# Kernel tuning notes

Hardware: AMD Instinct MI355X
Metric: run time of the kernel (lower is better)

## Reference

```python
import jax, jax.numpy as jnp
import numpy as np


def setup_inputs() -> dict:
    key = jax.random.key(0)
    k1, k2, k3, k4, k5 = jax.random.split(key, 5)
    B, S, T = 256, 512, 64
    emissions = jax.random.normal(k1, (B, S, T), dtype=jnp.float32)
    tags = jax.random.randint(k2, (B, S), 0, T, dtype=jnp.int64)
    mask = jnp.ones((B, S), dtype=jnp.int32)
    init_range = 0.1
    start_transitions = jax.random.uniform(k3, (T,), minval=-init_range, maxval=init_range, dtype=jnp.float32)
    end_transitions = jax.random.uniform(k4, (T,), minval=-init_range, maxval=init_range, dtype=jnp.float32)
    transitions = jax.random.uniform(k5, (T, T), minval=-init_range, maxval=init_range, dtype=jnp.float32)
    return {"emissions": emissions, "tags": tags, "mask": mask,
            "start_transitions": start_transitions,
            "end_transitions": end_transitions,
            "transitions": transitions}


def _crf_nll_mean(emissions, tags, mask, start_transitions, end_transitions, transitions):
    # batch_first -> time-major: [S, B, T], [S, B]
    em = jnp.transpose(emissions, (1, 0, 2))
    tg = jnp.transpose(tags, (1, 0))
    mk = jnp.transpose(mask, (1, 0))
    maskf = mk.astype(em.dtype)                      # [S, B]
    S, B, T = em.shape
    batch_idx = jnp.arange(B)

    # ---- numerator: score of the gold path (fully vectorized) ----
    emit = jnp.take_along_axis(em, tg[:, :, None], axis=2)[..., 0]   # [S, B]
    trans_sc = transitions[tg[:-1], tg[1:]]                          # [S-1, B]
    score_num = start_transitions[tg[0]] + emit[0]
    score_num = score_num + jnp.sum((trans_sc + emit[1:]) * maskf[1:], axis=0)
    seq_ends = jnp.sum(mk, axis=0) - 1                               # [B]
    last_tags = tg[seq_ends, batch_idx]
    score_num = score_num + end_transitions[last_tags]

    # ---- denominator: log-partition via logsumexp scan ----
    init = start_transitions + em[0]                                 # [B, T]

    def step(score, xs):
        em_i, m_i = xs                                               # [B,T], [B]
        # [B, T_prev, T_next]
        next_score = score[:, :, None] + transitions[None, :, :] + em_i[:, None, :]
        next_score = jax.nn.logsumexp(next_score, axis=1)
        score = jnp.where(m_i[:, None] != 0, next_score, score)
        return score, None

    final, _ = jax.lax.scan(step, init, (em[1:], mk[1:]))
    denom = jax.nn.logsumexp(final + end_transitions, axis=1)        # [B]

    llh = denom - score_num                                          # [B]
    return jnp.mean(llh)                                             # reduction='mean'


def reference(emissions, tags, mask, start_transitions, end_transitions, transitions):
    return _crf_nll_mean(emissions, tags, mask, start_transitions, end_transitions, transitions)
```

## Files before the change

### kernel.cpp

```cpp
#include <hip/hip_runtime.h>

#define BATCH 256
#define SEQ   512
#define NT    64
#define PITCH 68

typedef __attribute__((ext_vector_type(8)))  short bf16x8;
typedef __attribute__((ext_vector_type(16))) float f32x16;
typedef __attribute__((ext_vector_type(4)))  float f32x4;
typedef __attribute__((ext_vector_type(2)))  float f32x2;

static __device__ __forceinline__ unsigned pk_bf16(float lo, float hi) {
    return __builtin_amdgcn_perm(__float_as_uint(hi), __float_as_uint(lo), 0x07060302u);
}
static __device__ __forceinline__ short bf16_trunc(float v) {
    return (short)(__float_as_uint(v) >> 16);
}

template<int CLEN_>
struct slice_bytes {
    static constexpr int v = (CLEN_ * NT * 4 > 64 * PITCH * 2) ? CLEN_ * NT * 4 : 64 * PITCH * 2;
};

template<int PCH_, int CLEN_>
static __device__ __forceinline__ void chunk_wave(
    const float* __restrict__ emissions,
    const float* __restrict__ trans,
    unsigned short* __restrict__ mats,
    unsigned char* slice,
    int b, int c, int lane)
{
    float*          w_flat = (float*)slice;
    unsigned short* ldsT   = (unsigned short*)slice;

    const int h  = lane >> 5;
    const int ml = lane & 31;

    const int s0 = c * CLEN_;
    int L = (SEQ - 1) - s0; if (L > CLEN_) L = CLEN_;

    const float* em_b = emissions + (size_t)b * SEQ * NT;

    {
        const float4* src = (const float4*)(em_b + (size_t)(s0 + 1) * NT);
        float4*       dst = (float4*)w_flat;
        const int total4 = L * (NT / 4);
        for (int i = lane; i < total4; i += 64) {
            float4 v = src[i];
            v.x = __expf(v.x); v.y = __expf(v.y);
            v.z = __expf(v.z); v.w = __expf(v.w);
            dst[i] = v;
        }
    }

    bf16x8 Af[2][4];
#pragma unroll
    for (int mt = 0; mt < 2; ++mt) {
        int m = mt * 32 + ml;
#pragma unroll
        for (int kk = 0; kk < 4; ++kk) {
            bf16x8 f;
#pragma unroll
            for (int j = 0; j < 8; ++j) {
                int r = 32 * (kk >> 1) + 16 * (kk & 1) + (j & 3) + 8 * (j >> 2) + 4 * h;
                f[j] = bf16_trunc(__expf(trans[r * NT + m]) * 0.0078125f);
            }
            Af[mt][kk] = f;
        }
    }

    union BU { unsigned u[4]; bf16x8 v; };
    BU Bv[4][2];
#pragma unroll
    for (int kk = 0; kk < 4; ++kk)
#pragma unroll
        for (int nt = 0; nt < 2; ++nt) {
            int n = nt * 32 + ml;
#pragma unroll
            for (int d = 0; d < 4; ++d) {
                int j0 = 2 * d;
                int r0 = 32 * (kk >> 1) + 16 * (kk & 1) + (j0 & 3) + 8 * (j0 >> 2) + 4 * h;
                unsigned lo = (r0     == n) ? 0x3f80u : 0u;
                unsigned hi = (r0 + 1 == n) ? 0x3f80u : 0u;
                Bv[kk][nt].u[d] = lo | (hi << 16);
            }
        }

    __threadfence_block();

    const f32x16 zf = {};

    for (int s = 0; s < L; ++s) {
        const float* wrow = w_flat + s * NT;
        f32x4 wq[4][2];
#pragma unroll
        for (int kk = 0; kk < 4; ++kk) {
            int base = 32 * (kk >> 1) + 16 * (kk & 1) + 4 * h;
            wq[kk][0] = *(const f32x4*)(wrow + base);
            wq[kk][1] = *(const f32x4*)(wrow + base + 8);
        }

#pragma unroll
        for (int nt = 0; nt < 2; ++nt) {
            __builtin_amdgcn_s_setprio(1);
            f32x16 a0 = __builtin_amdgcn_mfma_f32_32x32x16_bf16(Af[0][0], Bv[0][nt].v, zf, 0, 0, 0);
            f32x16 a1 = __builtin_amdgcn_mfma_f32_32x32x16_bf16(Af[1][0], Bv[0][nt].v, zf, 0, 0, 0);
#pragma unroll
            for (int kk = 1; kk < 4; ++kk) {
                a0 = __builtin_amdgcn_mfma_f32_32x32x16_bf16(Af[0][kk], Bv[kk][nt].v, a0, 0, 0, 0);
                a1 = __builtin_amdgcn_mfma_f32_32x32x16_bf16(Af[1][kk], Bv[kk][nt].v, a1, 0, 0, 0);
            }
            __builtin_amdgcn_s_setprio(0);

#pragma unroll
            for (int kk = 0; kk < 4; ++kk) {
                const int qo = 8 * (kk & 1);
                const f32x4 wa = wq[kk][0], wb = wq[kk][1];
#pragma unroll
                for (int d = 0; d < 4; ++d) {
                    const int j0 = 2 * d;
                    float w0 = (d < 2) ? wa[j0]     : wb[j0 - 4];
                    float w1 = (d < 2) ? wa[j0 + 1] : wb[j0 - 3];
                    f32x2 av, wv;
                    if (kk < 2) { av[0] = a0[qo + j0]; av[1] = a0[qo + j0 + 1]; }
                    else        { av[0] = a1[qo + j0]; av[1] = a1[qo + j0 + 1]; }
                    wv[0] = w0; wv[1] = w1;
                    f32x2 p = av * wv;
                    Bv[kk][nt].u[d] = pk_bf16(p[0], p[1]);
                }
            }
        }
    }

    __threadfence_block();
#pragma unroll
    for (int kk = 0; kk < 4; ++kk)
#pragma unroll
        for (int nt = 0; nt < 2; ++nt) {
            int n = nt * 32 + ml;
#pragma unroll
            for (int d = 0; d < 4; ++d) {
                int j0 = 2 * d;
                int r0 = 32 * (kk >> 1) + 16 * (kk & 1) + (j0 & 3) + 8 * (j0 >> 2) + 4 * h;
                *(unsigned*)&ldsT[n * PITCH + r0] = Bv[kk][nt].u[d];
            }
        }
    __threadfence_block();

    unsigned short* outp = mats + ((size_t)(b * PCH_ + c)) * 4096;
    for (int it = 0; it < 8; ++it) {
        int o = it * 512 + lane * 8;
        int n = o >> 6, k = o & 63;
        const uint2* p = (const uint2*)(ldsT + n * PITCH + k);
        uint2 x = p[0], y = p[1];
        uint4 q4; q4.x = x.x; q4.y = x.y; q4.z = y.x; q4.w = y.y;
        *(uint4*)(outp + o) = q4;
    }
}

template<int PCH_, int CLEN_>
__global__ __launch_bounds__(256, 3) void crf_chunk_packed(
    const float* __restrict__ emissions,
    const float* __restrict__ trans,
    unsigned short* __restrict__ mats,
    float* __restrict__ ws_head)
{
    constexpr int SLICE_B = slice_bytes<CLEN_>::v;
    __shared__ __align__(16) unsigned char smem[4 * SLICE_B];

    const int tid  = threadIdx.x;
    const int lane = tid & 63;
    const int wave = tid >> 6;
    const int b    = blockIdx.y;
    const int c    = blockIdx.x * 4 + wave;

    if (blockIdx.x == 0 && b == 0 && tid == 0) {
        ws_head[0] = 0.f;
        ((unsigned*)ws_head)[1] = 0u;
    }

    chunk_wave<PCH_, CLEN_>(emissions, trans, mats, smem + wave * SLICE_B, b, c, lane);
}

template<int PCH_, int CLEN_>
__global__ __launch_bounds__(64, 3) void crf_chunk_kernel(
    const float* __restrict__ emissions,
    const float* __restrict__ trans,
    unsigned short* __restrict__ mats,
    float* __restrict__ ws_head)
{
    constexpr int SMEM = slice_bytes<CLEN_>::v;
    __shared__ __align__(16) unsigned char smem[SMEM];

    const int c    = blockIdx.x;
    const int b    = blockIdx.y;
    const int lane = threadIdx.x;

    if (c == 0 && b == 0 && lane == 0) {
        ws_head[0] = 0.f;
        ((unsigned*)ws_head)[1] = 0u;
    }

    chunk_wave<PCH_, CLEN_>(emissions, trans, mats, smem, b, c, lane);
}

template<int PCH_>
__global__ __launch_bounds__(256) void crf_combine_kernel(
    const float* __restrict__ emissions,
    const int*   __restrict__ tags,
    const int*   __restrict__ mask,
    const float* __restrict__ start_tr,
    const float* __restrict__ end_tr,
    const float* __restrict__ trans,
    const unsigned short* __restrict__ mats,
    float* __restrict__ ws_head,
    float* __restrict__ out)
{
    __shared__ __align__(16) float r_lds[NT];
    __shared__ float score_lds;

    const int b    = blockIdx.x;
    const int tid  = threadIdx.x;
    const int j    = tid & 63;
    const int wave = tid >> 6;

    const float* em_b = emissions + (size_t)b * SEQ * NT;
    const int*   tg_b = tags + b * SEQ;
    const int*   mk_b = mask + b * SEQ;
    const unsigned short* mb = mats + (size_t)b * PCH_ * 4096;

    float denom = 0.f;

    if (wave >= 2) {
        const uint4* p = (const uint4*)mb;
        unsigned acc = 0;
        for (int i = (wave - 2) * 64 + j; i < PCH_ * 512; i += 128) {
            uint4 q = p[i];
            acc += q.x + q.y + q.z + q.w;
        }
        if (acc == 0xdeadbeefu) ws_head[2] = -1.f;
    } else if (wave == 1) {
        float part = 0.f;
        int mcount = 0;
        for (int s = j; s < SEQ; s += 64) {
            int m = mk_b[s];
            mcount += m;
            int t = tg_b[s];
            if (s == 0) {
                part += start_tr[t] + em_b[t];
            } else {
                int tp = tg_b[s - 1];
                float v = trans[tp * NT + t] + em_b[s * NT + t];
                part += m ? v : 0.f;
            }
        }
#pragma unroll
        for (int d = 32; d; d >>= 1) {
            part   += __shfl_xor(part, d);
            mcount += __shfl_xor(mcount, d);
        }
        if (j == 0) score_lds = part + end_tr[tg_b[mcount - 1]];
    } else {
        float r = __expf(end_tr[j]);
        r_lds[j] = r;
        __threadfence_block();
        int X = 0;

        uint4 cur[8], nxt[8];
#pragma unroll
        for (int u = 0; u < 8; ++u)
            cur[u] = *(const uint4*)(mb + (size_t)(PCH_ - 1) * 4096 + j * 64 + u * 8);

        for (int c = PCH_ - 1; c >= 0; --c) {
            if (c > 0) {
#pragma unroll
                for (int u = 0; u < 8; ++u)
                    nxt[u] = *(const uint4*)(mb + (size_t)(c - 1) * 4096 + j * 64 + u * 8);
            }
            float a0 = 0.f, a1 = 0.f, a2 = 0.f, a3 = 0.f;
#pragma unroll
            for (int u = 0; u < 8; ++u) {
                uint4 q = cur[u];
                f32x4 ra = *(const f32x4*)&r_lds[u * 8];
                f32x4 rb = *(const f32x4*)&r_lds[u * 8 + 4];
                a0 = fmaf(ra[0], __uint_as_float(q.x << 16),         a0);
                a1 = fmaf(ra[1], __uint_as_float(q.x & 0xffff0000u), a1);
                a2 = fmaf(ra[2], __uint_as_float(q.y << 16),         a2);
                a3 = fmaf(ra[3], __uint_as_float(q.y & 0xffff0000u), a3);
                a0 = fmaf(rb[0], __uint_as_float(q.z << 16),         a0);
                a1 = fmaf(rb[1], __uint_as_float(q.z & 0xffff0000u), a1);
                a2 = fmaf(rb[2], __uint_as_float(q.w << 16),         a2);
                a3 = fmaf(rb[3], __uint_as_float(q.w & 0xffff0000u), a3);
            }
            float rn = (a0 + a1) + (a2 + a3);
            unsigned eb = (__builtin_amdgcn_readfirstlane((int)__float_as_uint(rn)) >> 23) & 0xffu;
            r = rn * __uint_as_float((254u - eb) << 23);
            X += (int)eb - 127;
            r_lds[j] = r;
            __threadfence_block();
#pragma unroll
            for (int u = 0; u < 8; ++u) cur[u] = nxt[u];
        }

        float u0 = __expf(start_tr[j] + em_b[j]);
        float v = r * u0;
#pragma unroll
        for (int d = 32; d; d >>= 1) v += __shfl_xor(v, d);
        denom = __logf(v) + (float)(X + 7 * (SEQ - 1)) * 0.6931471805599453f;
    }

    __syncthreads();

    if (wave == 0 && j == 0) {
        float llh = denom - score_lds;
        atomicAdd(&ws_head[0], llh * (1.0f / BATCH));
        __threadfence();
        unsigned old = atomicAdd((unsigned*)ws_head + 1, 1u);
        if (old == BATCH - 1) {
            __threadfence();
            out[0] = atomicAdd(&ws_head[0], 0.0f);
        }
    }
}

extern "C" void kernel_launch(void* const* d_in, const int* in_sizes, int n_in,
                              void* d_out, int out_size, void* d_ws, size_t ws_size,
                              hipStream_t stream) {
    const float* emissions = (const float*)d_in[0];
    const int*   tags      = (const int*)d_in[1];
    const int*   mask      = (const int*)d_in[2];
    const float* start_tr  = (const float*)d_in[3];
    const float* end_tr    = (const float*)d_in[4];
    const float* trans     = (const float*)d_in[5];

    float* ws_head = (float*)d_ws;
    unsigned short* mats = (unsigned short*)((char*)d_ws + 4096);

    const size_t need12 = 4096 + (size_t)BATCH * 12 * 4096 * sizeof(unsigned short);
    if (ws_size >= need12) {
        crf_chunk_packed<12, 43><<<dim3(3, BATCH), 256, 0, stream>>>(emissions, trans, mats, ws_head);
        crf_combine_kernel<12><<<BATCH, 256, 0, stream>>>(emissions, tags, mask,
                                                          start_tr, end_tr, trans, mats,
                                                          ws_head, (float*)d_out);
    } else {
        crf_chunk_kernel<8, 64><<<dim3(8, BATCH), 64, 0, stream>>>(emissions, trans, mats, ws_head);
        crf_combine_kernel<8><<<BATCH, 256, 0, stream>>>(emissions, tags, mask,
                                                         start_tr, end_tr, trans, mats,
                                                         ws_head, (float*)d_out);
    }
}
```

Measured before the change: 151.0 us.

## Split each chunk's column halves across two waves with 8 chunks

Each sequence chunk's 64x64 transfer-matrix product is now split across two waves, each owning one 32-column half (nt), instead of one wave doing both halves. Chunk count changes from 12 chunks of 43 steps to 8 chunks of 64 steps, and the small-workspace fallback path is removed. This halves the serial MFMA/elementwise work per wave per step to shorten the latency-bound chain, at the cost of longer chunks, added __syncthreads, and a larger grid of waves.

```diff
diff --git a/kernel.cpp b/kernel.cpp
--- a/kernel.cpp
+++ b/kernel.cpp
@@ -23,12 +23,12 @@
 };
 
 template<int PCH_, int CLEN_>
-static __device__ __forceinline__ void chunk_wave(
+static __device__ __forceinline__ void chunk_wave_half(
     const float* __restrict__ emissions,
     const float* __restrict__ trans,
     unsigned short* __restrict__ mats,
     unsigned char* slice,
-    int b, int c, int lane)
+    int b, int c, int nt, int lane)
 {
     float*          w_flat = (float*)slice;
     unsigned short* ldsT   = (unsigned short*)slice;
@@ -45,7 +45,7 @@
         const float4* src = (const float4*)(em_b + (size_t)(s0 + 1) * NT);
         float4*       dst = (float4*)w_flat;
         const int total4 = L * (NT / 4);
-        for (int i = lane; i < total4; i += 64) {
+        for (int i = nt * 64 + lane; i < total4; i += 128) {
             float4 v = src[i];
             v.x = __expf(v.x); v.y = __expf(v.y);
             v.z = __expf(v.z); v.w = __expf(v.w);
@@ -70,23 +70,22 @@
     }
 
     union BU { unsigned u[4]; bf16x8 v; };
-    BU Bv[4][2];
-#pragma unroll
-    for (int kk = 0; kk < 4; ++kk)
-#pragma unroll
-        for (int nt = 0; nt < 2; ++nt) {
-            int n = nt * 32 + ml;
+    BU Bv[4];
+    {
+        int n = nt * 32 + ml;
+#pragma unroll
+        for (int kk = 0; kk < 4; ++kk)
 #pragma unroll
             for (int d = 0; d < 4; ++d) {
                 int j0 = 2 * d;
                 int r0 = 32 * (kk >> 1) + 16 * (kk & 1) + (j0 & 3) + 8 * (j0 >> 2) + 4 * h;
                 unsigned lo = (r0     == n) ? 0x3f80u : 0u;
                 unsigned hi = (r0 + 1 == n) ? 0x3f80u : 0u;
-                Bv[kk][nt].u[d] = lo | (hi << 16);
-            }
-        }
-
-    __threadfence_block();
+                Bv[kk].u[d] = lo | (hi << 16);
+            }
+    }
+
+    __syncthreads();
 
     const f32x16 zf = {};
 
@@ -100,56 +99,52 @@
             wq[kk][1] = *(const f32x4*)(wrow + base + 8);
         }
 
-#pragma unroll
-        for (int nt = 0; nt < 2; ++nt) {
-            __builtin_amdgcn_s_setprio(1);
-            f32x16 a0 = __builtin_amdgcn_mfma_f32_32x32x16_bf16(Af[0][0], Bv[0][nt].v, zf, 0, 0, 0);
-            f32x16 a1 = __builtin_amdgcn_mfma_f32_32x32x16_bf16(Af[1][0], Bv[0][nt].v, zf, 0, 0, 0);
-#pragma unroll
-            for (int kk = 1; kk < 4; ++kk) {
-                a0 = __builtin_amdgcn_mfma_f32_32x32x16_bf16(Af[0][kk], Bv[kk][nt].v, a0, 0, 0, 0);
-                a1 = __builtin_amdgcn_mfma_f32_32x32x16_bf16(Af[1][kk], Bv[kk][nt].v, a1, 0, 0, 0);
-            }
-            __builtin_amdgcn_s_setprio(0);
-
-#pragma unroll
-            for (int kk = 0; kk < 4; ++kk) {
-                const int qo = 8 * (kk & 1);
-                const f32x4 wa = wq[kk][0], wb = wq[kk][1];
-#pragma unroll
-                for (int d = 0; d < 4; ++d) {
-                    const int j0 = 2 * d;
-                    float w0 = (d < 2) ? wa[j0]     : wb[j0 - 4];
-                    float w1 = (d < 2) ? wa[j0 + 1] : wb[j0 - 3];
-                    f32x2 av, wv;
-                    if (kk < 2) { av[0] = a0[qo + j0]; av[1] = a0[qo + j0 + 1]; }
-                    else        { av[0] = a1[qo + j0]; av[1] = a1[qo + j0 + 1]; }
-                    wv[0] = w0; wv[1] = w1;
-                    f32x2 p = av * wv;
-                    Bv[kk][nt].u[d] = pk_bf16(p[0], p[1]);
-                }
-            }
-        }
-    }
-
-    __threadfence_block();
-#pragma unroll
-    for (int kk = 0; kk < 4; ++kk)
-#pragma unroll
-        for (int nt = 0; nt < 2; ++nt) {
-            int n = nt * 32 + ml;
+        __builtin_amdgcn_s_setprio(1);
+        f32x16 a0 = __builtin_amdgcn_mfma_f32_32x32x16_bf16(Af[0][0], Bv[0].v, zf, 0, 0, 0);
+        f32x16 a1 = __builtin_amdgcn_mfma_f32_32x32x16_bf16(Af[1][0], Bv[0].v, zf, 0, 0, 0);
+#pragma unroll
+        for (int kk = 1; kk < 4; ++kk) {
+            a0 = __builtin_amdgcn_mfma_f32_32x32x16_bf16(Af[0][kk], Bv[kk].v, a0, 0, 0, 0);
+            a1 = __builtin_amdgcn_mfma_f32_32x32x16_bf16(Af[1][kk], Bv[kk].v, a1, 0, 0, 0);
+        }
+        __builtin_amdgcn_s_setprio(0);
+
+#pragma unroll
+        for (int kk = 0; kk < 4; ++kk) {
+            const int qo = 8 * (kk & 1);
+            const f32x4 wa = wq[kk][0], wb = wq[kk][1];
+#pragma unroll
+            for (int d = 0; d < 4; ++d) {
+                const int j0 = 2 * d;
+                float w0 = (d < 2) ? wa[j0]     : wb[j0 - 4];
+                float w1 = (d < 2) ? wa[j0 + 1] : wb[j0 - 3];
+                f32x2 av, wv;
+                if (kk < 2) { av[0] = a0[qo + j0]; av[1] = a0[qo + j0 + 1]; }
+                else        { av[0] = a1[qo + j0]; av[1] = a1[qo + j0 + 1]; }
+                wv[0] = w0; wv[1] = w1;
+                f32x2 p = av * wv;
+                Bv[kk].u[d] = pk_bf16(p[0], p[1]);
+            }
+        }
+    }
+
+    __syncthreads();
+    {
+        int n = nt * 32 + ml;
+#pragma unroll
+        for (int kk = 0; kk < 4; ++kk)
 #pragma unroll
             for (int d = 0; d < 4; ++d) {
                 int j0 = 2 * d;
                 int r0 = 32 * (kk >> 1) + 16 * (kk & 1) + (j0 & 3) + 8 * (j0 >> 2) + 4 * h;
-                *(unsigned*)&ldsT[n * PITCH + r0] = Bv[kk][nt].u[d];
-            }
-        }
+                *(unsigned*)&ldsT[n * PITCH + r0] = Bv[kk].u[d];
+            }
+    }
     __threadfence_block();
 
     unsigned short* outp = mats + ((size_t)(b * PCH_ + c)) * 4096;
-    for (int it = 0; it < 8; ++it) {
-        int o = it * 512 + lane * 8;
+    for (int it = 0; it < 4; ++it) {
+        int o = nt * 2048 + it * 512 + lane * 8;
         int n = o >> 6, k = o & 63;
         const uint2* p = (const uint2*)(ldsT + n * PITCH + k);
         uint2 x = p[0], y = p[1];
@@ -159,49 +154,29 @@
 }
 
 template<int PCH_, int CLEN_>
-__global__ __launch_bounds__(256, 3) void crf_chunk_packed(
+__global__ __launch_bounds__(256, 4) void crf_chunk_split(
     const float* __restrict__ emissions,
     const float* __restrict__ trans,
     unsigned short* __restrict__ mats,
     float* __restrict__ ws_head)
 {
-    constexpr int SLICE_B = slice_bytes<CLEN_>::v;
-    __shared__ __align__(16) unsigned char smem[4 * SLICE_B];
+    constexpr int SLICE_CH = slice_bytes<CLEN_>::v;
+    __shared__ __align__(16) unsigned char smem[2 * SLICE_CH];
 
     const int tid  = threadIdx.x;
     const int lane = tid & 63;
-    const int wave = tid >> 6;
+    const int w    = tid >> 6;
     const int b    = blockIdx.y;
-    const int c    = blockIdx.x * 4 + wave;
+    const int c    = blockIdx.x * 2 + (w >> 1);
+    const int nt   = w & 1;
 
     if (blockIdx.x == 0 && b == 0 && tid == 0) {
         ws_head[0] = 0.f;
         ((unsigned*)ws_head)[1] = 0u;
     }
 
-    chunk_wave<PCH_, CLEN_>(emissions, trans, mats, smem + wave * SLICE_B, b, c, lane);
-}
-
-template<int PCH_, int CLEN_>
-__global__ __launch_bounds__(64, 3) void crf_chunk_kernel(
-    const float* __restrict__ emissions,
-    const float* __restrict__ trans,
-    unsigned short* __restrict__ mats,
-    float* __restrict__ ws_head)
-{
-    constexpr int SMEM = slice_bytes<CLEN_>::v;
-    __shared__ __align__(16) unsigned char smem[SMEM];
-
-    const int c    = blockIdx.x;
-    const int b    = blockIdx.y;
-    const int lane = threadIdx.x;
-
-    if (c == 0 && b == 0 && lane == 0) {
-        ws_head[0] = 0.f;
-        ((unsigned*)ws_head)[1] = 0u;
-    }
-
-    chunk_wave<PCH_, CLEN_>(emissions, trans, mats, smem, b, c, lane);
+    chunk_wave_half<PCH_, CLEN_>(emissions, trans, mats,
+                                 smem + (w >> 1) * SLICE_CH, b, c, nt, lane);
 }
 
 template<int PCH_>
@@ -336,16 +311,8 @@
     float* ws_head = (float*)d_ws;
     unsigned short* mats = (unsigned short*)((char*)d_ws + 4096);
 
-    const size_t need12 = 4096 + (size_t)BATCH * 12 * 4096 * sizeof(unsigned short);
-    if (ws_size >= need12) {
-        crf_chunk_packed<12, 43><<<dim3(3, BATCH), 256, 0, stream>>>(emissions, trans, mats, ws_head);
-        crf_combine_kernel<12><<<BATCH, 256, 0, stream>>>(emissions, tags, mask,
-                                                          start_tr, end_tr, trans, mats,
-                                                          ws_head, (float*)d_out);
-    } else {
-        crf_chunk_kernel<8, 64><<<dim3(8, BATCH), 64, 0, stream>>>(emissions, trans, mats, ws_head);
-        crf_combine_kernel<8><<<BATCH, 256, 0, stream>>>(emissions, tags, mask,
-                                                         start_tr, end_tr, trans, mats,
-                                                         ws_head, (float*)d_out);
-    }
-}
+    crf_chunk_split<8, 64><<<dim3(4, BATCH), 256, 0, stream>>>(emissions, trans, mats, ws_head);
+    crf_combine_kernel<8><<<BATCH, 256, 0, stream>>>(emissions, tags, mask,
+                                                     start_tr, end_tr, trans, mats,
+                                                     ws_head, (float*)d_out);
+}
```

Measured after the change: 150.4 us. Within noise of the previous version (-0.4%).
